# Kernel optimization log

Measured on AMD Instinct MI355X. Metric: run time of the kernel, lower is better.

The kernel has to match this reference:

```python
import jax, jax.numpy as jnp
import numpy as np

C = 1000        # class_num
D = 128         # feature_dim
N = 2_000_000   # number of samples
MOMENTUM = 0.9


def setup_inputs() -> dict:
    key = jax.random.key(0)
    k1, k2, k3 = jax.random.split(key, 3)
    features = jax.random.normal(k1, (N, D), dtype=jnp.float32)
    labels = jax.random.randint(k2, (N,), 0, C)
    prototypes = jax.random.normal(k3, (C, D), dtype=jnp.float32)
    prototypes = prototypes.at[: C // 10].set(0.0)
    return {"features": features, "labels": labels, "prototypes": prototypes}


def reference(features, labels, prototypes):
    # Fused scatter-mean over classes: one O(N) pass instead of a C-way loop.
    sums = jax.ops.segment_sum(features, labels, num_segments=C)          # [C, D]
    counts = jax.ops.segment_sum(
        jnp.ones((features.shape[0],), dtype=features.dtype), labels, num_segments=C
    )                                                                      # [C]
    mean = sums / jnp.maximum(counts, 1.0)[:, None]                        # [C, D]

    has_samples = (counts > 0)[:, None]                                    # class seen in batch
    is_uninit = (jnp.sum(prototypes, axis=1) == 0.0)[:, None]              # prototypes[i].sum()==0
    ema = MOMENTUM * prototypes + (1.0 - MOMENTUM) * mean
    new_prototypes = jnp.where(has_samples, jnp.where(is_uninit, mean, ema), prototypes)
    return new_prototypes
```

## Files before the change

kernel.cpp:

```cpp
#include <hip/hip_runtime.h>

#define C_NUM 1000
#define D_DIM 128
#define MOMENTUM 0.9f
#define KCHUNKS 32
#define NBLK 1024
#define SLICE 256


__global__ __launch_bounds__(256) void chunk_hist_kernel(
        const int* __restrict__ labels, int n, int* __restrict__ mat) {
    __shared__ int h[C_NUM];
    int b = blockIdx.x;
    int chunk = (n + NBLK - 1) / NBLK;
    int start = b * chunk, end = min(start + chunk, n);
    for (int i = threadIdx.x; i < C_NUM; i += 256) h[i] = 0;
    __syncthreads();
    for (int i = start + threadIdx.x; i < end; i += 256)
        atomicAdd(&h[labels[i]], 1);
    __syncthreads();
    for (int c = threadIdx.x; c < C_NUM; c += 256)
        mat[c * NBLK + b] = h[c];
}

__global__ __launch_bounds__(256) void scan_mat_kernel(
        int* __restrict__ mat, int* __restrict__ counts) {
    __shared__ int ts[256];
    int c = blockIdx.x;
    int t = threadIdx.x;
    int* row = mat + c * NBLK;
    int4 v = ((int4*)row)[t];
    int s0 = v.x, s1 = s0 + v.y, s2 = s1 + v.z, s3 = s2 + v.w;
    ts[t] = s3;
    __syncthreads();
    for (int d = 1; d < 256; d <<= 1) {
        int val = (t >= d) ? ts[t - d] : 0;
        __syncthreads();
        ts[t] += val;
        __syncthreads();
    }
    int base = (t > 0) ? ts[t - 1] : 0;
    int4 o;
    o.x = base;
    o.y = base + s0;
    o.z = base + s1;
    o.w = base + s2;
    ((int4*)row)[t] = o;
    if (t == 255) counts[c] = ts[255];
}

__global__ void scan_offsets_kernel(const int* __restrict__ counts,
                                    int* __restrict__ offsets) {
    __shared__ int s[1024];
    int t = threadIdx.x;
    int c = (t < C_NUM) ? counts[t] : 0;
    s[t] = c;
    __syncthreads();
    for (int d = 1; d < 1024; d <<= 1) {
        int v = (t >= d) ? s[t - d] : 0;
        __syncthreads();
        s[t] += v;
        __syncthreads();
    }
    if (t < C_NUM) offsets[t] = s[t] - c;
}

__global__ __launch_bounds__(256) void place_kernel(
        const int* __restrict__ labels, int n,
        const int* __restrict__ mat, const int* __restrict__ offsets,
        int* __restrict__ order) {
    __shared__ int cur[C_NUM];
    int b = blockIdx.x;
    int chunk = (n + NBLK - 1) / NBLK;
    int start = b * chunk, end = min(start + chunk, n);
    for (int c = threadIdx.x; c < C_NUM; c += 256)
        cur[c] = offsets[c] + mat[c * NBLK + b];
    __syncthreads();
    for (int i = start + threadIdx.x; i < end; i += 256) {
        int lab = labels[i];
        int pos = atomicAdd(&cur[lab], 1);
        order[pos] = i;
    }
}

__global__ __launch_bounds__(256) void partial_reduce_kernel(
        const float4* __restrict__ feat4, const int* __restrict__ order,
        const int* __restrict__ counts, const int* __restrict__ offsets,
        float* __restrict__ sums_part) {
    int c = blockIdx.x >> 5;
    int k = blockIdx.x & (KCHUNKS - 1);
    int cnt = counts[c];
    int off = offsets[c];
    int len = (cnt + KCHUNKS - 1) / KCHUNKS;
    int start = off + k * len;
    int end = min(start + len, off + cnt);

    int tid = threadIdx.x;
    int sub = tid >> 5;
    int q = tid & 31;

    __shared__ int ord[SLICE];
    float4 acc = make_float4(0.f, 0.f, 0.f, 0.f);

    for (int base = start; base < end; base += SLICE) {
        int m = min(SLICE, end - base);
        if (tid < m) ord[tid] = order[base + tid];
        __syncthreads();
        int i = sub;
        for (; i + 24 < m; i += 32) {
            int r0 = ord[i], r1 = ord[i + 8], r2 = ord[i + 16], r3 = ord[i + 24];
            float4 v0 = feat4[(long)r0 * 32 + q];
            float4 v1 = feat4[(long)r1 * 32 + q];
            float4 v2 = feat4[(long)r2 * 32 + q];
            float4 v3 = feat4[(long)r3 * 32 + q];
            acc.x += (v0.x + v1.x) + (v2.x + v3.x);
            acc.y += (v0.y + v1.y) + (v2.y + v3.y);
            acc.z += (v0.z + v1.z) + (v2.z + v3.z);
            acc.w += (v0.w + v1.w) + (v2.w + v3.w);
        }
        for (; i < m; i += 8) {
            int r = ord[i];
            float4 v = feat4[(long)r * 32 + q];
            acc.x += v.x; acc.y += v.y; acc.z += v.z; acc.w += v.w;
        }
        __syncthreads();
    }

    __shared__ float4 lds4[256];
    lds4[tid] = acc;
    __syncthreads();
    if (tid < D_DIM) {
        const float* lds = (const float*)lds4;
        float s = 0.f;
        #pragma unroll
        for (int g = 0; g < 8; ++g) s += lds[g * D_DIM + tid];
        sums_part[((long)k * C_NUM + c) * D_DIM + tid] = s;
    }
}

__global__ __launch_bounds__(128) void finalize_slices_kernel(
        const float* __restrict__ prototypes, const float* __restrict__ sums_part,
        const int* __restrict__ counts, float* __restrict__ out) {
    __shared__ float red[D_DIM];
    int c = blockIdx.x, d = threadIdx.x;
    float s = 0.f;
    #pragma unroll 8
    for (int k = 0; k < KCHUNKS; ++k)
        s += sums_part[((long)k * C_NUM + c) * D_DIM + d];
    float proto = prototypes[c * D_DIM + d];
    red[d] = proto;
    __syncthreads();
    for (int t = 64; t > 0; t >>= 1) {
        if (d < t) red[d] += red[d + t];
        __syncthreads();
    }
    float rowsum = red[0];
    int cnt = counts[c];
    float mean = s / (float)max(cnt, 1);
    float ema = MOMENTUM * proto + (1.f - MOMENTUM) * mean;
    out[c * D_DIM + d] = (cnt > 0) ? ((rowsum == 0.f) ? mean : ema) : proto;
}

__global__ void zero_ws_words_kernel(int* __restrict__ ws, int n) {
    int i = blockIdx.x * blockDim.x + threadIdx.x;
    if (i < n) ws[i] = 0;
}

__global__ void hist_kernel(const int* __restrict__ labels, int n,
                            int* __restrict__ counts) {
    __shared__ int h[C_NUM];
    for (int i = threadIdx.x; i < C_NUM; i += blockDim.x) h[i] = 0;
    __syncthreads();
    int idx = blockIdx.x * blockDim.x + threadIdx.x;
    int stride = gridDim.x * blockDim.x;
    for (int i = idx; i < n; i += stride) atomicAdd(&h[labels[i]], 1);
    __syncthreads();
    for (int i = threadIdx.x; i < C_NUM; i += blockDim.x) {
        int v = h[i];
        if (v) atomicAdd(&counts[i], v);
    }
}

__global__ void scatter_kernel(const float4* __restrict__ feat4,
                               const int* __restrict__ labels,
                               float* __restrict__ sums, long total4) {
    long idx = (long)blockIdx.x * blockDim.x + threadIdx.x;
    long stride = (long)gridDim.x * blockDim.x;
    for (long i = idx; i < total4; i += stride) {
        float4 v = feat4[i];
        int row = (int)(i >> 5);
        int q = (int)(i & 31);
        int lab = labels[row];
        float* dst = sums + lab * D_DIM + q * 4;
        atomicAdd(dst + 0, v.x);
        atomicAdd(dst + 1, v.y);
        atomicAdd(dst + 2, v.z);
        atomicAdd(dst + 3, v.w);
    }
}

__global__ void finalize_kernel(const float* __restrict__ prototypes,
                                const float* __restrict__ sums,
                                const int* __restrict__ counts,
                                float* __restrict__ out) {
    __shared__ float red[D_DIM];
    int c = blockIdx.x;
    int d = threadIdx.x;
    float proto = prototypes[c * D_DIM + d];
    red[d] = proto;
    __syncthreads();
    for (int s = 64; s > 0; s >>= 1) {
        if (d < s) red[d] += red[d + s];
        __syncthreads();
    }
    float rowsum = red[0];
    int cnt = counts[c];
    float mean = sums[c * D_DIM + d] / (float)max(cnt, 1);
    float ema = MOMENTUM * proto + (1.0f - MOMENTUM) * mean;
    out[c * D_DIM + d] = (cnt > 0) ? ((rowsum == 0.0f) ? mean : ema) : proto;
}

extern "C" void kernel_launch(void* const* d_in, const int* in_sizes, int n_in,
                              void* d_out, int out_size, void* d_ws, size_t ws_size,
                              hipStream_t stream) {
    const float* features   = (const float*)d_in[0];
    const int*   labels     = (const int*)d_in[1];
    const float* prototypes = (const float*)d_in[2];
    float* out = (float*)d_out;
    int n = in_sizes[1];

    int* counts     = (int*)d_ws;
    int* offsets    = counts + C_NUM;
    int* mat        = offsets + C_NUM;
    float* sums_part = (float*)(mat + (size_t)C_NUM * NBLK);
    int* order      = (int*)(sums_part + (size_t)KCHUNKS * C_NUM * D_DIM);

    size_t need = ((size_t)2 * C_NUM + (size_t)C_NUM * NBLK +
                   (size_t)KCHUNKS * C_NUM * D_DIM + (size_t)n) * sizeof(int);
    if (ws_size >= need) {
        chunk_hist_kernel<<<NBLK, 256, 0, stream>>>(labels, n, mat);
        scan_mat_kernel<<<C_NUM, 256, 0, stream>>>(mat, counts);
        scan_offsets_kernel<<<1, 1024, 0, stream>>>(counts, offsets);
        place_kernel<<<NBLK, 256, 0, stream>>>(labels, n, mat, offsets, order);
        partial_reduce_kernel<<<C_NUM * KCHUNKS, 256, 0, stream>>>(
            (const float4*)features, order, counts, offsets, sums_part);
        finalize_slices_kernel<<<C_NUM, D_DIM, 0, stream>>>(
            prototypes, sums_part, counts, out);
    } else {
        float* fsums = (float*)d_ws;
        int* fcounts = (int*)(fsums + C_NUM * D_DIM);
        int zero_n = C_NUM * D_DIM + C_NUM;
        zero_ws_words_kernel<<<(zero_n + 255) / 256, 256, 0, stream>>>((int*)d_ws, zero_n);
        hist_kernel<<<512, 256, 0, stream>>>(labels, n, fcounts);
        long total4 = (long)n * (D_DIM / 4);
        scatter_kernel<<<2048, 256, 0, stream>>>((const float4*)features, labels, fsums, total4);
        finalize_kernel<<<C_NUM, D_DIM, 0, stream>>>(prototypes, fsums, fcounts, out);
    }
}
```

Baseline: 264.1 us.

## Stage per-block counting-sort placement in shared memory with fewer larger chunks

Reduces the histogram block count to 256 and replaces direct atomic-cursor scatter with a shared-memory staged placement: each block re-histograms its chunk, scans locally, sorts indices into LDS, then writes contiguous per-class runs to the global order array. The aim is more coalesced writes of the order array and a smaller block-by-class matrix to scan. In exchange it adds a second histogram pass, a per-element binary search, large LDS use and lower block-level parallelism; a global-atomic fallback covers large chunks.

```diff
diff --git a/kernel.cpp b/kernel.cpp
--- a/kernel.cpp
+++ b/kernel.cpp
@@ -4,7 +4,8 @@
 #define D_DIM 128
 #define MOMENTUM 0.9f
 #define KCHUNKS 32
-#define NBLK 1024
+#define NBLK 256
+#define STAGE_MAX 7936
 #define SLICE 256
 
 
@@ -25,28 +26,21 @@
 
 __global__ __launch_bounds__(256) void scan_mat_kernel(
         int* __restrict__ mat, int* __restrict__ counts) {
-    __shared__ int ts[256];
+    __shared__ int s[NBLK];
     int c = blockIdx.x;
     int t = threadIdx.x;
     int* row = mat + c * NBLK;
-    int4 v = ((int4*)row)[t];
-    int s0 = v.x, s1 = s0 + v.y, s2 = s1 + v.z, s3 = s2 + v.w;
-    ts[t] = s3;
-    __syncthreads();
-    for (int d = 1; d < 256; d <<= 1) {
-        int val = (t >= d) ? ts[t - d] : 0;
-        __syncthreads();
-        ts[t] += val;
-        __syncthreads();
-    }
-    int base = (t > 0) ? ts[t - 1] : 0;
-    int4 o;
-    o.x = base;
-    o.y = base + s0;
-    o.z = base + s1;
-    o.w = base + s2;
-    ((int4*)row)[t] = o;
-    if (t == 255) counts[c] = ts[255];
+    int v = row[t];
+    s[t] = v;
+    __syncthreads();
+    for (int d = 1; d < NBLK; d <<= 1) {
+        int val = (t >= d) ? s[t - d] : 0;
+        __syncthreads();
+        s[t] += val;
+        __syncthreads();
+    }
+    row[t] = s[t] - v;
+    if (t == NBLK - 1) counts[c] = s[NBLK - 1];
 }
 
 __global__ void scan_offsets_kernel(const int* __restrict__ counts,
@@ -65,20 +59,81 @@
     if (t < C_NUM) offsets[t] = s[t] - c;
 }
 
-__global__ __launch_bounds__(256) void place_kernel(
+__global__ __launch_bounds__(256) void place_staged_kernel(
         const int* __restrict__ labels, int n,
         const int* __restrict__ mat, const int* __restrict__ offsets,
         int* __restrict__ order) {
-    __shared__ int cur[C_NUM];
+    __shared__ int h[1024];
+    __shared__ int loc[1028];
+    __shared__ int gbase[C_NUM];
+    __shared__ int ps[256];
+    __shared__ int stage[STAGE_MAX];
     int b = blockIdx.x;
+    int t = threadIdx.x;
     int chunk = (n + NBLK - 1) / NBLK;
     int start = b * chunk, end = min(start + chunk, n);
-    for (int c = threadIdx.x; c < C_NUM; c += 256)
-        cur[c] = offsets[c] + mat[c * NBLK + b];
-    __syncthreads();
-    for (int i = start + threadIdx.x; i < end; i += 256) {
+    int m = end - start;
+
+    for (int i = t; i < 1024; i += 256) h[i] = 0;
+    for (int c = t; c < C_NUM; c += 256)
+        gbase[c] = offsets[c] + mat[c * NBLK + b];
+    __syncthreads();
+    for (int i = start + t; i < end; i += 256)
+        atomicAdd(&h[labels[i]], 1);
+    __syncthreads();
+
+    int c4 = t * 4;
+    int a0 = h[c4], a1 = h[c4 + 1], a2 = h[c4 + 2], a3 = h[c4 + 3];
+    int ssum = a0 + a1 + a2 + a3;
+    ps[t] = ssum;
+    __syncthreads();
+    for (int d = 1; d < 256; d <<= 1) {
+        int v = (t >= d) ? ps[t - d] : 0;
+        __syncthreads();
+        ps[t] += v;
+        __syncthreads();
+    }
+    int excl = ps[t] - ssum;
+    loc[c4]     = excl;
+    loc[c4 + 1] = excl + a0;
+    loc[c4 + 2] = excl + a0 + a1;
+    loc[c4 + 3] = excl + a0 + a1 + a2;
+    __syncthreads();
+
+    for (int c = t; c < C_NUM; c += 256) h[c] = loc[c];
+    __syncthreads();
+
+    for (int i = start + t; i < end; i += 256) {
         int lab = labels[i];
-        int pos = atomicAdd(&cur[lab], 1);
+        int p = atomicAdd(&h[lab], 1);
+        stage[p] = i;
+    }
+    __syncthreads();
+
+    for (int j = t; j < m; j += 256) {
+        int lo = 0, hi = C_NUM - 1;
+        while (lo < hi) {
+            int mid = (lo + hi + 1) >> 1;
+            if (loc[mid] <= j) lo = mid; else hi = mid - 1;
+        }
+        order[gbase[lo] + (j - loc[lo])] = stage[j];
+    }
+}
+
+__global__ void init_cursor_kernel(const int* __restrict__ offsets,
+                                   int* __restrict__ cursor) {
+    int i = blockIdx.x * blockDim.x + threadIdx.x;
+    if (i < C_NUM) cursor[i] = offsets[i];
+}
+
+__global__ void build_order_kernel(const int* __restrict__ labels, int n,
+                                   int* __restrict__ cursor,
+                                   int* __restrict__ order) {
+    int idx = blockIdx.x * blockDim.x + threadIdx.x;
+    int stride = gridDim.x * blockDim.x;
+    for (int i = idx; i < n; i += stride) {
+        int lab = labels[i];
+        int pos = atomicAdd(&cursor[lab], 1);
         order[pos] = i;
     }
 }
@@ -229,19 +284,26 @@
     float* out = (float*)d_out;
     int n = in_sizes[1];
 
-    int* counts     = (int*)d_ws;
-    int* offsets    = counts + C_NUM;
-    int* mat        = offsets + C_NUM;
+    int* counts      = (int*)d_ws;
+    int* offsets     = counts + C_NUM;
+    int* cursor      = offsets + C_NUM;
+    int* mat         = cursor + C_NUM;
     float* sums_part = (float*)(mat + (size_t)C_NUM * NBLK);
-    int* order      = (int*)(sums_part + (size_t)KCHUNKS * C_NUM * D_DIM);
-
-    size_t need = ((size_t)2 * C_NUM + (size_t)C_NUM * NBLK +
+    int* order       = (int*)(sums_part + (size_t)KCHUNKS * C_NUM * D_DIM);
+
+    size_t need = ((size_t)3 * C_NUM + (size_t)C_NUM * NBLK +
                    (size_t)KCHUNKS * C_NUM * D_DIM + (size_t)n) * sizeof(int);
     if (ws_size >= need) {
+        int chunk = (n + NBLK - 1) / NBLK;
         chunk_hist_kernel<<<NBLK, 256, 0, stream>>>(labels, n, mat);
-        scan_mat_kernel<<<C_NUM, 256, 0, stream>>>(mat, counts);
+        scan_mat_kernel<<<C_NUM, NBLK, 0, stream>>>(mat, counts);
         scan_offsets_kernel<<<1, 1024, 0, stream>>>(counts, offsets);
-        place_kernel<<<NBLK, 256, 0, stream>>>(labels, n, mat, offsets, order);
+        if (chunk <= STAGE_MAX) {
+            place_staged_kernel<<<NBLK, 256, 0, stream>>>(labels, n, mat, offsets, order);
+        } else {
+            init_cursor_kernel<<<(C_NUM + 255) / 256, 256, 0, stream>>>(offsets, cursor);
+            build_order_kernel<<<1024, 256, 0, stream>>>(labels, n, cursor, order);
+        }
         partial_reduce_kernel<<<C_NUM * KCHUNKS, 256, 0, stream>>>(
             (const float4*)features, order, counts, offsets, sums_part);
         finalize_slices_kernel<<<C_NUM, D_DIM, 0, stream>>>(
```

New measurement: 269.2 us. Within noise of the previous version (+1.9%).
